# Optimization experiments

Measured on AMD Instinct MI355X. Metric: run time of the kernel, lower is better.

The kernel has to match this reference:

```python
import jax, jax.numpy as jnp
import numpy as np

N, E, D, R = 50000, 800000, 128, 200


def setup_inputs() -> dict:
    key = jax.random.key(0)
    ks = jax.random.split(key, 8)
    h = jax.random.normal(ks[0], (N, D), jnp.float32)
    emb_rel = jax.random.normal(ks[1], (R, D), jnp.float32)
    loop_weight = jax.random.normal(ks[2], (D, D), jnp.float32) * 0.05
    attn_fc_w = jax.random.normal(ks[3], (D, 3 * D), jnp.float32) * 0.05  # Linear(3D,D) weight [D,3D]
    attn_fc2_w = jax.random.normal(ks[4], (1, D), jnp.float32) * 0.05     # Linear(D,1) weight [1,D]
    src = jax.random.randint(ks[5], (E,), 0, N)
    dst = jax.random.randint(ks[6], (E,), 0, N)
    etype = jax.random.randint(ks[7], (E,), 0, R)
    return {"h": h, "emb_rel": emb_rel, "loop_weight": loop_weight,
            "attn_fc_w": attn_fc_w, "attn_fc2_w": attn_fc2_w,
            "src": src, "dst": dst, "etype": etype}


def reference(h, emb_rel, loop_weight, attn_fc_w, attn_fc2_w, src, dst, etype):
    num_nodes = h.shape[0]
    # attn_fc(concat([h_src, h_dst, rel])) == h_src@Ws.T + h_dst@Wd.T + rel@Wr.T
    # (avoids materializing the [E, 3D] concat)
    Ws, Wd, Wr = jnp.split(attn_fc_w, 3, axis=1)  # each [D, D]
    hs = h[src]  # [E, D] gathered source features
    a = hs @ Ws.T + h[dst] @ Wd.T + emb_rel[etype] @ Wr.T  # [E, D]
    e = jax.nn.leaky_relu((a @ attn_fc2_w.T)[:, 0], 0.01)  # [E] edge logits
    # segment softmax over destination node (stable)
    m = jax.ops.segment_max(e, dst, num_segments=num_nodes)
    w = jnp.exp(e - m[dst])
    denom = jax.ops.segment_sum(w, dst, num_segments=num_nodes)
    alpha = w / denom[dst]  # [E]
    # weighted scatter-sum of source features into destination nodes
    agg = jax.ops.segment_sum(alpha[:, None] * hs, dst, num_segments=num_nodes)
    # DGL update_all leaves zero-in-degree nodes' feature unchanged
    deg = jax.ops.segment_sum(jnp.ones_like(e), dst, num_segments=num_nodes)
    agg = jnp.where(deg[:, None] > 0, agg, h)
    # self-loop message
    return agg + h @ loop_weight
```

## Files before the change

kernel.cpp:

```cpp
#include <hip/hip_runtime.h>

#define D 128
#define TD 384

__global__ void k_prep(const float* __restrict__ A, const float* __restrict__ v,
                       float* __restrict__ p) {
  __shared__ float vs[D];
  int t = threadIdx.x;
  if (t < D) vs[t] = v[t];
  __syncthreads();
  float acc = 0.f;
#pragma unroll 8
  for (int i = 0; i < D; ++i) acc += vs[i] * A[i * TD + t];
  p[t] = acc;
}

__global__ void k_scores_hist(const float* __restrict__ h, const float* __restrict__ emb,
                              const float* __restrict__ p, const int* __restrict__ dst,
                              float* __restrict__ ss, float* __restrict__ sd,
                              float* __restrict__ sr, int* __restrict__ cnt,
                              int N, int R, int E, int nbScore) {
  int t = threadIdx.x;
  if ((int)blockIdx.x < nbScore) {
    __shared__ float pl[TD];
    pl[t] = p[t];
    if (t < TD - 256) pl[256 + t] = p[256 + t];
    __syncthreads();
    int w = blockIdx.x * 4 + (t >> 6);
    int l = t & 63;
    if (w < N) {
      float x0 = h[(size_t)w * D + l];
      float x1 = h[(size_t)w * D + 64 + l];
      float a = x0 * pl[l] + x1 * pl[64 + l];
      float b = x0 * pl[128 + l] + x1 * pl[192 + l];
#pragma unroll
      for (int o = 32; o; o >>= 1) { a += __shfl_xor(a, o); b += __shfl_xor(b, o); }
      if (l == 0) { ss[w] = a; sd[w] = b; }
    } else if (w < N + R) {
      int r = w - N;
      float x0 = emb[(size_t)r * D + l];
      float x1 = emb[(size_t)r * D + 64 + l];
      float c = x0 * pl[256 + l] + x1 * pl[320 + l];
#pragma unroll
      for (int o = 32; o; o >>= 1) c += __shfl_xor(c, o);
      if (l == 0) sr[r] = c;
    }
  } else {
    int i = (blockIdx.x - nbScore) * 256 + t;
    int stride = (gridDim.x - nbScore) * 256;
    for (; i < E; i += stride) atomicAdd(&cnt[dst[i]], 1);
  }
}

__global__ void k_scan1(int* __restrict__ cnt, int* __restrict__ bsum, int N) {
  __shared__ int wsum[16];
  int t = threadIdx.x, lane = t & 63, wid = t >> 6;
  int i = blockIdx.x * 1024 + t;
  int v = (i < N) ? cnt[i] : 0;
  int x = v;
#pragma unroll
  for (int o = 1; o < 64; o <<= 1) {
    int y = __shfl_up(x, o);
    if (lane >= o) x += y;
  }
  if (lane == 63) wsum[wid] = x;
  __syncthreads();
  if (t < 16) {
    int y = wsum[t];
#pragma unroll
    for (int o = 1; o < 16; o <<= 1) {
      int z = __shfl_up(y, o);
      if (t >= o) y += z;
    }
    wsum[t] = y;
  }
  __syncthreads();
  int woff = wid ? wsum[wid - 1] : 0;
  if (i < N) cnt[i] = woff + x - v;
  if (t == 0) bsum[blockIdx.x] = wsum[15];
}

__global__ void k_scan2(int* __restrict__ bsum, int nsb) {
  int l = threadIdx.x;
  int v = (l < nsb) ? bsum[l] : 0;
  int x = v;
#pragma unroll
  for (int o = 1; o < 64; o <<= 1) {
    int y = __shfl_up(x, o);
    if (l >= o) x += y;
  }
  if (l < nsb) bsum[l] = x - v;
}

__global__ void k_scan3(const int* __restrict__ bsum, int* __restrict__ cnt,
                        int* __restrict__ cur, int N, int E) {
  int i = blockIdx.x * 1024 + threadIdx.x;
  if (i < N) {
    int v = cnt[i] + bsum[blockIdx.x];
    cnt[i] = v;
    cur[i] = v;
  }
  if (i == 0) cnt[N] = E;
}

__global__ void k_edge(const int* __restrict__ src, const int* __restrict__ dst,
                       const int* __restrict__ et, const float* __restrict__ ss,
                       const float* __restrict__ sd, const float* __restrict__ sr,
                       int* __restrict__ cur, float* __restrict__ esort,
                       int* __restrict__ ssort, int E) {
  int i = blockIdx.x * blockDim.x + threadIdx.x;
  if (i >= E) return;
  int s = src[i], d = dst[i], r = et[i];
  float e = ss[s] + sd[d] + sr[r];
  e = (e > 0.f) ? e : 0.01f * e;
  int pos = atomicAdd(&cur[d], 1);
  esort[pos] = e;
  ssort[pos] = s;
}

__global__ __launch_bounds__(128) void k_agg(const float* __restrict__ h,
                                             const int* __restrict__ off,
                                             const float* __restrict__ esort,
                                             const int* __restrict__ ssort,
                                             float* __restrict__ out, int N) {
  int n = blockIdx.x;
  int t = threadIdx.x;
  int start = off[n], end = off[n + 1];
  int deg = end - start;
  if (deg == 0) {
    out[(size_t)n * D + t] = h[(size_t)n * D + t];
    return;
  }
  int lane = t & 63, wid = t >> 6;
  __shared__ float mred[2];
  __shared__ float sred[2];
  __shared__ float wch[128];
  __shared__ int sch[128];

  float m = -3.4e38f;
  for (int i = t; i < deg; i += 128) m = fmaxf(m, esort[start + i]);
#pragma unroll
  for (int o = 32; o; o >>= 1) m = fmaxf(m, __shfl_xor(m, o));
  if (lane == 0) mred[wid] = m;
  __syncthreads();
  m = fmaxf(mred[0], mred[1]);

  float acc = 0.f;
  float wpriv = 0.f;
  for (int cs = 0; cs < deg; cs += 128) {
    int cn = min(128, deg - cs);
    __syncthreads();
    if (t < cn) {
      float w = __expf(esort[start + cs + t] - m);
      wpriv += w;
      wch[t] = w;
      sch[t] = ssort[start + cs + t];
    }
    __syncthreads();
#pragma unroll 4
    for (int i = 0; i < cn; ++i) acc += wch[i] * h[(size_t)sch[i] * D + t];
  }
#pragma unroll
  for (int o = 32; o; o >>= 1) wpriv += __shfl_xor(wpriv, o);
  if (lane == 0) sred[wid] = wpriv;
  __syncthreads();
  float denom = sred[0] + sred[1];
  out[(size_t)n * D + t] = acc / denom;
}

__global__ __launch_bounds__(128) void k_final(const float* __restrict__ h,
                                               const float* __restrict__ lw,
                                               float* __restrict__ out, int N) {
  int j = threadIdx.x;
  float w[D];
#pragma unroll
  for (int k = 0; k < D; ++k) w[k] = lw[(size_t)k * D + j];
  for (int n = blockIdx.x; n < N; n += gridDim.x) {
    const float4* __restrict__ hr4 =
        reinterpret_cast<const float4*>(h + (size_t)n * D);
    float acc = 0.f;
#pragma unroll
    for (int q = 0; q < D / 4; ++q) {
      float4 hv = hr4[q];
      acc = fmaf(hv.x, w[4 * q + 0], acc);
      acc = fmaf(hv.y, w[4 * q + 1], acc);
      acc = fmaf(hv.z, w[4 * q + 2], acc);
      acc = fmaf(hv.w, w[4 * q + 3], acc);
    }
    out[(size_t)n * D + j] += acc;
  }
}

extern "C" void kernel_launch(void* const* d_in, const int* in_sizes, int n_in,
                              void* d_out, int out_size, void* d_ws, size_t ws_size,
                              hipStream_t stream) {
  const float* h   = (const float*)d_in[0];
  const float* emb = (const float*)d_in[1];
  const float* lw  = (const float*)d_in[2];
  const float* afw = (const float*)d_in[3];
  const float* af2 = (const float*)d_in[4];
  const int* src = (const int*)d_in[5];
  const int* dst = (const int*)d_in[6];
  const int* et  = (const int*)d_in[7];
  int N = in_sizes[0] / D;
  int R = in_sizes[1] / D;
  int E = in_sizes[5];
  float* out = (float*)d_out;

  char* ws = (char*)d_ws;
  size_t o = 0;
  auto alloc = [&](size_t bytes) -> void* {
    void* pp = ws + o;
    o = (o + bytes + 255) & ~(size_t)255;
    return pp;
  };
  float* p     = (float*)alloc((size_t)TD * 4);
  float* ss    = (float*)alloc((size_t)N * 4);
  float* sd    = (float*)alloc((size_t)N * 4);
  float* srel  = (float*)alloc((size_t)R * 4);
  int*   cnt   = (int*)  alloc((size_t)(N + 1) * 4);
  int*   cur   = (int*)  alloc((size_t)N * 4);
  int*   bsum  = (int*)  alloc((size_t)64 * 4);
  float* esort = (float*)alloc((size_t)E * 4);
  int*   ssort = (int*)  alloc((size_t)E * 4);

  int nsb = (N + 1023) / 1024;

  hipMemsetAsync(cnt, 0, (size_t)(N + 1) * 4, stream);
  k_prep<<<1, TD, 0, stream>>>(afw, af2, p);
  int nbScore = (N + R + 3) / 4;
  int nbHist = 2048;
  k_scores_hist<<<nbScore + nbHist, 256, 0, stream>>>(h, emb, p, dst, ss, sd, srel,
                                                      cnt, N, R, E, nbScore);
  k_scan1<<<nsb, 1024, 0, stream>>>(cnt, bsum, N);
  k_scan2<<<1, 64, 0, stream>>>(bsum, nsb);
  k_scan3<<<nsb, 1024, 0, stream>>>(bsum, cnt, cur, N, E);
  k_edge<<<(E + 255) / 256, 256, 0, stream>>>(src, dst, et, ss, sd, srel, cur,
                                              esort, ssort, E);
  k_agg<<<N, 128, 0, stream>>>(h, cnt, esort, ssort, out, N);
  k_final<<<2048, 128, 0, stream>>>(h, lw, out, N);
}
```

Measured before the change: 334.5 us.

## Parallelize aggregation over edge slots with float4 loads; unroll two rows in self-loop GEMV

k_agg now uses 256 threads as 8 edge slots of 32 float4 lanes. Each slot computes its own weights and gathers neighbour rows independently, and the slot partials are reduced in shared memory. This removes the per-chunk barriers and the serial loop over edges, so more gathers are in flight per node. k_final processes two rows per iteration with split accumulators, pins the weights in registers, uses launch bounds (128,2) and a halved grid, which raises ILP but keeps register pressure high.

```diff
diff --git a/kernel.cpp b/kernel.cpp
--- a/kernel.cpp
+++ b/kernel.cpp
@@ -118,76 +118,108 @@
   ssort[pos] = s;
 }
 
-__global__ __launch_bounds__(128) void k_agg(const float* __restrict__ h,
+__global__ __launch_bounds__(256) void k_agg(const float* __restrict__ h,
                                              const int* __restrict__ off,
                                              const float* __restrict__ esort,
                                              const int* __restrict__ ssort,
                                              float* __restrict__ out, int N) {
   int n = blockIdx.x;
   int t = threadIdx.x;
-  int start = off[n], end = off[n + 1];
-  int deg = end - start;
+  int start = off[n], deg = off[n + 1] - start;
+  int qc = t & 31;
+  int slot = t >> 5;
   if (deg == 0) {
-    out[(size_t)n * D + t] = h[(size_t)n * D + t];
+    if (slot == 0)
+      ((float4*)(out + (size_t)n * D))[qc] = ((const float4*)(h + (size_t)n * D))[qc];
     return;
   }
-  int lane = t & 63, wid = t >> 6;
-  __shared__ float mred[2];
-  __shared__ float sred[2];
-  __shared__ float wch[128];
-  __shared__ int sch[128];
+  __shared__ float4 part[8][32];
+  __shared__ float dpart[8];
+  __shared__ float mred[4];
 
   float m = -3.4e38f;
-  for (int i = t; i < deg; i += 128) m = fmaxf(m, esort[start + i]);
+  for (int i = t; i < deg; i += 256) m = fmaxf(m, esort[start + i]);
 #pragma unroll
   for (int o = 32; o; o >>= 1) m = fmaxf(m, __shfl_xor(m, o));
-  if (lane == 0) mred[wid] = m;
-  __syncthreads();
-  m = fmaxf(mred[0], mred[1]);
-
-  float acc = 0.f;
+  if ((t & 63) == 0) mred[t >> 6] = m;
+  __syncthreads();
+  m = fmaxf(fmaxf(mred[0], mred[1]), fmaxf(mred[2], mred[3]));
+
+  float4 acc = {0.f, 0.f, 0.f, 0.f};
   float wpriv = 0.f;
-  for (int cs = 0; cs < deg; cs += 128) {
-    int cn = min(128, deg - cs);
-    __syncthreads();
-    if (t < cn) {
-      float w = __expf(esort[start + cs + t] - m);
-      wpriv += w;
-      wch[t] = w;
-      sch[t] = ssort[start + cs + t];
-    }
-    __syncthreads();
-#pragma unroll 4
-    for (int i = 0; i < cn; ++i) acc += wch[i] * h[(size_t)sch[i] * D + t];
-  }
-#pragma unroll
-  for (int o = 32; o; o >>= 1) wpriv += __shfl_xor(wpriv, o);
-  if (lane == 0) sred[wid] = wpriv;
-  __syncthreads();
-  float denom = sred[0] + sred[1];
-  out[(size_t)n * D + t] = acc / denom;
-}
-
-__global__ __launch_bounds__(128) void k_final(const float* __restrict__ h,
-                                               const float* __restrict__ lw,
-                                               float* __restrict__ out, int N) {
+  for (int i = slot; i < deg; i += 8) {
+    float w = __expf(esort[start + i] - m);
+    int s = ssort[start + i];
+    float4 hv = ((const float4*)(h + (size_t)s * D))[qc];
+    acc.x = fmaf(w, hv.x, acc.x);
+    acc.y = fmaf(w, hv.y, acc.y);
+    acc.z = fmaf(w, hv.z, acc.z);
+    acc.w = fmaf(w, hv.w, acc.w);
+    wpriv += w;
+  }
+  part[slot][qc] = acc;
+  if (qc == 0) dpart[slot] = wpriv;
+  __syncthreads();
+  if (slot == 0) {
+    float4 s4 = part[0][qc];
+#pragma unroll
+    for (int s2 = 1; s2 < 8; ++s2) {
+      float4 p4 = part[s2][qc];
+      s4.x += p4.x; s4.y += p4.y; s4.z += p4.z; s4.w += p4.w;
+    }
+    float denom = ((dpart[0] + dpart[1]) + (dpart[2] + dpart[3])) +
+                  ((dpart[4] + dpart[5]) + (dpart[6] + dpart[7]));
+    float inv = 1.f / denom;
+    float4 r;
+    r.x = s4.x * inv; r.y = s4.y * inv; r.z = s4.z * inv; r.w = s4.w * inv;
+    ((float4*)(out + (size_t)n * D))[qc] = r;
+  }
+}
+
+__global__ __launch_bounds__(128, 2) void k_final(const float* __restrict__ h,
+                                                  const float* __restrict__ lw,
+                                                  float* __restrict__ out, int N) {
   int j = threadIdx.x;
   float w[D];
 #pragma unroll
   for (int k = 0; k < D; ++k) w[k] = lw[(size_t)k * D + j];
-  for (int n = blockIdx.x; n < N; n += gridDim.x) {
-    const float4* __restrict__ hr4 =
-        reinterpret_cast<const float4*>(h + (size_t)n * D);
-    float acc = 0.f;
-#pragma unroll
-    for (int q = 0; q < D / 4; ++q) {
-      float4 hv = hr4[q];
-      acc = fmaf(hv.x, w[4 * q + 0], acc);
-      acc = fmaf(hv.y, w[4 * q + 1], acc);
-      acc = fmaf(hv.z, w[4 * q + 2], acc);
-      acc = fmaf(hv.w, w[4 * q + 3], acc);
-    }
-    out[(size_t)n * D + j] += acc;
+#pragma unroll
+  for (int k = 0; k < D; ++k) asm volatile("" : "+v"(w[k]));
+
+  int stride = gridDim.x;
+  for (int n = blockIdx.x; n < N; n += 2 * stride) {
+    int n2 = n + stride;
+    const float4* __restrict__ ra = (const float4*)(h + (size_t)n * D);
+    float a0 = 0.f, a1 = 0.f, a2 = 0.f, a3 = 0.f;
+    float b0 = 0.f, b1 = 0.f, b2 = 0.f, b3 = 0.f;
+    if (n2 < N) {
+      const float4* __restrict__ rb = (const float4*)(h + (size_t)n2 * D);
+#pragma unroll
+      for (int q = 0; q < D / 4; ++q) {
+        float4 va = ra[q];
+        float4 vb = rb[q];
+        a0 = fmaf(va.x, w[4 * q + 0], a0);
+        a1 = fmaf(va.y, w[4 * q + 1], a1);
+        a2 = fmaf(va.z, w[4 * q + 2], a2);
+        a3 = fmaf(va.w, w[4 * q + 3], a3);
+        b0 = fmaf(vb.x, w[4 * q + 0], b0);
+        b1 = fmaf(vb.y, w[4 * q + 1], b1);
+        b2 = fmaf(vb.z, w[4 * q + 2], b2);
+        b3 = fmaf(vb.w, w[4 * q + 3], b3);
+      }
+      out[(size_t)n * D + j] += (a0 + a1) + (a2 + a3);
+      out[(size_t)n2 * D + j] += (b0 + b1) + (b2 + b3);
+    } else {
+#pragma unroll
+      for (int q = 0; q < D / 4; ++q) {
+        float4 va = ra[q];
+        a0 = fmaf(va.x, w[4 * q + 0], a0);
+        a1 = fmaf(va.y, w[4 * q + 1], a1);
+        a2 = fmaf(va.z, w[4 * q + 2], a2);
+        a3 = fmaf(va.w, w[4 * q + 3], a3);
+      }
+      out[(size_t)n * D + j] += (a0 + a1) + (a2 + a3);
+    }
   }
 }
 
@@ -237,6 +269,6 @@
   k_scan3<<<nsb, 1024, 0, stream>>>(bsum, cnt, cur, N, E);
   k_edge<<<(E + 255) / 256, 256, 0, stream>>>(src, dst, et, ss, sd, srel, cur,
                                               esort, ssort, E);
-  k_agg<<<N, 128, 0, stream>>>(h, cnt, esort, ssort, out, N);
-  k_final<<<2048, 128, 0, stream>>>(h, lw, out, N);
-}
+  k_agg<<<N, 256, 0, stream>>>(h, cnt, esort, ssort, out, N);
+  k_final<<<1024, 128, 0, stream>>>(h, lw, out, N);
+}
```

Result: slower. 356.1 us (+6.4%).
